# Performance work log

Hardware: AMD Instinct MI355X
Metric: run time of the kernel (lower is better)

## Reference

```python
import jax, jax.numpy as jnp
import numpy as np

N = 100000      # total nodes (100 graphs x 1000 nodes each)
G = 100         # graphs per batch
F_IN = 12       # node_features (temporal window)
F_OUT = 32      # DCRNN hidden size (hardcoded in module)
K = 5           # diffusion (Chebyshev) steps (hardcoded)
C = 4           # num_classes
E = 16 * N      # edges: ring (N) + random (15N)


def setup_inputs() -> dict:
    key = jax.random.key(0)
    ks = jax.random.split(key, 12)
    x = jax.random.normal(ks[0], (N, F_IN), dtype=jnp.float32)
    ring = jnp.arange(N, dtype=jnp.int32)
    src = jnp.concatenate([ring, jax.random.randint(ks[1], (15 * N,), 0, N, dtype=jnp.int32)])
    dst = jnp.concatenate([(ring + 1) % N, jax.random.randint(ks[2], (15 * N,), 0, N, dtype=jnp.int32)])
    edge_index = jnp.stack([src, dst])  # [2, E]
    edge_weight = jax.random.uniform(ks[3], (E,), dtype=jnp.float32, minval=0.1, maxval=1.0)
    batch = (jnp.arange(N, dtype=jnp.int32) * G) // N  # sorted graph ids, 1000 nodes per graph
    s = 0.1
    return dict(
        x=x, edge_index=edge_index, edge_weight=edge_weight, batch=batch,
        W_z=jax.random.normal(ks[4], (2, K, F_IN + F_OUT, F_OUT), jnp.float32) * s,
        b_z=jax.random.normal(ks[5], (F_OUT,), jnp.float32) * s,
        W_r=jax.random.normal(ks[6], (2, K, F_IN + F_OUT, F_OUT), jnp.float32) * s,
        b_r=jax.random.normal(ks[7], (F_OUT,), jnp.float32) * s,
        W_h=jax.random.normal(ks[8], (2, K, F_IN + F_OUT, F_OUT), jnp.float32) * s,
        b_h=jax.random.normal(ks[9], (F_OUT,), jnp.float32) * s,
        W_lin=jax.random.normal(ks[10], (F_OUT, C), jnp.float32) * s,
        b_lin=jax.random.normal(ks[11], (C,), jnp.float32) * s,
    )


def reference(x, edge_index, edge_weight, batch, W_z, b_z, W_r, b_r, W_h, b_h, W_lin, b_lin):
    row, col = edge_index[0], edge_index[1]
    # weighted in/out degrees (to_dense_adj sums duplicate edges, same as segment_sum)
    deg_out_inv = 1.0 / jax.ops.segment_sum(edge_weight, row, num_segments=N)
    deg_in_inv = 1.0 / jax.ops.segment_sum(edge_weight, col, num_segments=N)
    norm_out = deg_out_inv[row][:, None]  # per-edge 1/deg_out(src)
    norm_in = deg_in_inv[row][:, None]    # per-edge 1/deg_in(src), as in DConv

    def prop_fwd(h):  # out[dst] += h[src]/deg_out[src]
        return jax.ops.segment_sum(norm_out * h[row], col, num_segments=N)

    def prop_rev(h):  # reverse (transposed) diffusion: out[src] += h[dst]/deg_in[src]
        return jax.ops.segment_sum(norm_in * h[col], row, num_segments=N)

    def dconv(Xc, W, b):
        # Chebyshev diffusion conv, W: [2, K, F_in+F_out, F_out]
        H = Xc @ (W[0, 0] + W[1, 0])
        T1o, T1i = prop_fwd(Xc), prop_rev(Xc)
        H = H + T1o @ W[0, 1] + T1i @ W[1, 1]
        T0o = T0i = Xc
        for k in range(2, K):
            T2o = 2.0 * prop_fwd(T1o) - T0o
            T2i = 2.0 * prop_rev(T1i) - T0i
            H = H + T2o @ W[0, k] + T2i @ W[1, k]
            T0o, T1o = T1o, T2o
            T0i, T1i = T1i, T2i
        return H + b

    # GRU gating with zero-initialized hidden state (H=None in module)
    Hst = jnp.zeros((N, F_OUT), x.dtype)
    XH = jnp.concatenate([x, Hst], axis=1)
    Z = jax.nn.sigmoid(dconv(XH, W_z, b_z))
    R = jax.nn.sigmoid(dconv(XH, W_r, b_r))
    XRH = jnp.concatenate([x, R * Hst], axis=1)
    H_tilde = jnp.tanh(dconv(XRH, W_h, b_h))
    H = Z * Hst + (1.0 - Z) * H_tilde

    h = jax.nn.relu(H) @ W_lin + b_lin            # [N, C]
    sums = jax.ops.segment_sum(h, batch, num_segments=G)
    counts = jax.ops.segment_sum(jnp.ones((N,), h.dtype), batch, num_segments=G)
    return sums / counts[:, None]                 # global_mean_pool -> [G, C]
```

## Files before the change

kernel.cpp:

```cpp
#include <hip/hip_runtime.h>
#include <math.h>

#define NN    100000
#define GG    100
#define FIN   12
#define FOUT  32
#define KD    5
#define CC    4
#define EE    1600000
#define ROWS  108
#define NBF   782
#define NBINS 1564
#define NBC   256
#define CHUNK 6250
#define NSEG  (NBINS * NBC)

__device__ __forceinline__ unsigned bfr(float f) {
    unsigned u = __float_as_uint(f);
    return (u + 0x7FFFu + ((u >> 16) & 1u)) >> 16;
}
__device__ __forceinline__ unsigned pack2(float a, float b) {
    return bfr(a) | (bfr(b) << 16);
}
#define BLO(u) __uint_as_float((u) << 16)
#define BHI(u) __uint_as_float((u) & 0xFFFF0000u)

__device__ __forceinline__ int chunk_of_block(int b) {
    return ((b & 7) << 5) | (b >> 3);
}


__global__ __launch_bounds__(512) void k_hist(const int* __restrict__ ei,
                                              int* __restrict__ hist_g) {
    __shared__ int hist[NBINS];
    for (int i = threadIdx.x; i < NBINS; i += 512) hist[i] = 0;
    __syncthreads();
    int chunk = chunk_of_block(blockIdx.x);
    int lo = chunk * CHUNK, hi = lo + CHUNK;
    if (hi > EE) hi = EE;
    for (int e = lo + threadIdx.x; e < hi; e += 512) {
        int s = ei[e], d = ei[EE + e];
        atomicAdd(&hist[d >> 7], 1);
        atomicAdd(&hist[NBF + (s >> 7)], 1);
    }
    __syncthreads();
    for (int i = threadIdx.x; i < NBINS; i += 512)
        hist_g[i * NBC + chunk] = hist[i];
}

__global__ __launch_bounds__(1024) void k_scan1(int* __restrict__ g,
                                                int* __restrict__ bsum) {
    __shared__ int sh[1024];
    int t = threadIdx.x;
    int i = blockIdx.x * 1024 + t;
    int v = g[i];
    sh[t] = v;
    __syncthreads();
    for (int d = 1; d < 1024; d <<= 1) {
        int x = sh[t];
        if (t >= d) x += sh[t - d];
        __syncthreads();
        sh[t] = x;
        __syncthreads();
    }
    g[i] = sh[t] - v;
    if (t == 1023) bsum[blockIdx.x] = sh[1023];
}

__global__ __launch_bounds__(1024) void k_scan2(int* __restrict__ bsum, int nb) {
    __shared__ int sh[1024];
    int t = threadIdx.x;
    int a = (2 * t     < nb) ? bsum[2 * t]     : 0;
    int b = (2 * t + 1 < nb) ? bsum[2 * t + 1] : 0;
    int s = a + b;
    sh[t] = s;
    __syncthreads();
    for (int d = 1; d < 1024; d <<= 1) {
        int x = sh[t];
        if (t >= d) x += sh[t - d];
        __syncthreads();
        sh[t] = x;
        __syncthreads();
    }
    int base = sh[t] - s;
    if (2 * t < nb)     bsum[2 * t] = base;
    if (2 * t + 1 < nb) bsum[2 * t + 1] = base + a;
}

__global__ __launch_bounds__(1024) void k_scan3(int* __restrict__ g,
                                                const int* __restrict__ bsum,
                                                int* __restrict__ off,
                                                int* __restrict__ off_node) {
    int i = blockIdx.x * 1024 + threadIdx.x;
    int v = g[i] + bsum[blockIdx.x];
    g[i] = v;
    if ((i & (NBC - 1)) == 0) off[i / NBC] = v;
    if (i == 0) { off[NBINS] = 2 * EE; off_node[2 * NN] = 2 * EE; }
}

__global__ __launch_bounds__(512) void k_place(const int* __restrict__ ei,
                                               const float* __restrict__ ew,
                                               const int* __restrict__ base_g,
                                               int2* __restrict__ recA) {
    __shared__ int cur[NBINS];
    int chunk = chunk_of_block(blockIdx.x);
    for (int i = threadIdx.x; i < NBINS; i += 512) cur[i] = base_g[i * NBC + chunk];
    __syncthreads();
    int lo = chunk * CHUNK, hi = lo + CHUNK;
    if (hi > EE) hi = EE;
    for (int e = lo + threadIdx.x; e < hi; e += 512) {
        int s = ei[e], d = ei[EE + e];
        float w = ew[e];
        int pf = atomicAdd(&cur[d >> 7], 1);
        recA[pf] = make_int2(s | ((d & 127) << 17), __float_as_int(w));
        int pr = atomicAdd(&cur[NBF + (s >> 7)], 1);
        recA[pr] = make_int2(d | ((s & 127) << 17), __float_as_int(w));
    }
}

__global__ __launch_bounds__(256) void k_subcsr(
        const int* __restrict__ off, const int2* __restrict__ recA,
        const float* __restrict__ x,
        int* __restrict__ off_node, int* __restrict__ rec2,
        float* __restrict__ dinv_in, float* __restrict__ dinv_out,
        uint2* __restrict__ gA) {
    __shared__ int   hist[128];
    __shared__ int   lofs[128];
    __shared__ int   cur[128];
    __shared__ float wsum[128];
    __shared__ float dl[128];
    int b = blockIdx.x;
    int t = threadIdx.x;
    if (t < 128) { hist[t] = 0; wsum[t] = 0.f; }
    __syncthreads();
    int e0 = off[b], e1 = off[b + 1];
    for (int e = e0 + t; e < e1; e += 256) {
        int2 r = recA[e];
        int loc = r.x >> 17;
        atomicAdd(&hist[loc], 1);
        atomicAdd(&wsum[loc], __int_as_float(r.y));
    }
    __syncthreads();
    if (t < 128) lofs[t] = hist[t];
    __syncthreads();
    for (int d = 1; d < 128; d <<= 1) {
        int v = 0;
        if (t < 128 && t >= d) v = lofs[t - d];
        __syncthreads();
        if (t < 128) lofs[t] += v;
        __syncthreads();
    }
    bool rev = b >= NBF;
    int base = (rev ? b - NBF : b) * 128;
    if (t < 128) {
        int ex = lofs[t] - hist[t];
        lofs[t] = ex;
        cur[t] = 0;
        int node = base + t;
        if (node < NN) {
            off_node[(rev ? NN : 0) + node] = e0 + ex;
            float inv = 1.f / wsum[t];
            dl[t] = inv;
            if (rev) dinv_out[node] = inv;
            else     dinv_in[node]  = inv;
        }
    }
    __syncthreads();
    for (int e = e0 + t; e < e1; e += 256) {
        int rx = recA[e].x;
        int loc = rx >> 17;
        int pos = e0 + lofs[loc] + atomicAdd(&cur[loc], 1);
        rec2[pos] = rx & 0x1FFFF;
    }
    if (rev) {
        __syncthreads();
        for (int i = t; i < 128 * 3; i += 256) {
            int loc = i / 3, cc = i - loc * 3;
            int node = base + loc;
            if (node < NN) {
                float4 v = *(const float4*)(x + (size_t)node * FIN + cc * 4);
                float sc = dl[loc];
                gA[(size_t)node * 3 + cc] =
                    make_uint2(pack2(v.x * sc, v.y * sc), pack2(v.z * sc, v.w * sc));
            }
        }
    }
}


__global__ void k_misc(const float* __restrict__ Wz_in, const float* __restrict__ Wh_in,
                       float* __restrict__ Wz, float* __restrict__ Wh,
                       const float* __restrict__ b_lin, float* __restrict__ out,
                       const float* __restrict__ x, uint2* __restrict__ xb) {
    int t = blockIdx.x * 256 + threadIdx.x;
    if (t < 2 * ROWS * FOUT) {
        int sel = t / (ROWS * FOUT);
        int rem = t - sel * ROWS * FOUT;
        int r = rem / FOUT;
        int f = rem - r * FOUT;
        int b = r / 12;
        int i = r - b * 12;
        const float* Ws = sel ? Wh_in : Wz_in;
        float v;
        if (b == 0)
            v = Ws[(0 * KD + 0) * 44 * 32 + i * 32 + f] + Ws[(1 * KD + 0) * 44 * 32 + i * 32 + f];
        else if (b <= 4)
            v = Ws[(0 * KD + b) * 44 * 32 + i * 32 + f];
        else
            v = Ws[(1 * KD + (b - 4)) * 44 * 32 + i * 32 + f];
        (sel ? Wh : Wz)[r * FOUT + f] = v;
    }
    int u = t - 2 * ROWS * FOUT;
    if (u >= 0 && u < GG * CC) out[u] = b_lin[u & 3];
    if (t < 3 * NN) {
        int n = t / 3, c = t - n * 3;
        float4 v = *(const float4*)(x + (size_t)n * FIN + c * 4);
        xb[(size_t)n * 3 + c] = make_uint2(pack2(v.x, v.y), pack2(v.z, v.w));
    }
}

#define LREC 2048
__global__ __launch_bounds__(256) void k_gather(
        const int* __restrict__ off_node, const int* __restrict__ rec2,
        const uint2* __restrict__ gIn, const uint2* __restrict__ hIn,
        const uint2* __restrict__ prevF, const uint2* __restrict__ prevR,
        const float* __restrict__ dinv_in, const float* __restrict__ dinv_out,
        uint2* __restrict__ outF, uint2* __restrict__ outR,
        uint2* __restrict__ gOut, float c) {
    __shared__ int lrec[LREC];
    int xcd = blockIdx.x & 7;
    int grp = blockIdx.x >> 3;
    bool rev = xcd >= 4;
    int dbase = rev ? NN : 0;
    int ub = (grp * 4 + (xcd & 3)) * 256;
    int lin = ub + threadIdx.x;

    int u1 = ub + 255; if (u1 > 3 * NN - 1) u1 = 3 * NN - 1;
    int node0 = ub / 3, node1 = u1 / 3;
    int w0 = off_node[dbase + node0];
    int w1 = off_node[dbase + node1 + 1];
    int wn = w1 - w0;
    bool useLds = (wn <= LREC);
    if (useLds) {
        for (int i = threadIdx.x; i < wn; i += 256) lrec[i] = rec2[w0 + i];
    }
    __syncthreads();

    if (lin < 3 * NN) {
        int node = lin / 3;
        int ch = lin - node * 3;
        int i0 = dbase + node;
        int e0 = off_node[i0], e1 = off_node[i0 + 1];
        const uint2* in = rev ? hIn : gIn;

        float ax = 0.f, ay = 0.f, az = 0.f, aw = 0.f;
        float bx = 0.f, by = 0.f, bz = 0.f, bw = 0.f;
        if (useLds) {
            int a0 = e0 - w0, a1 = e1 - w0;
            int e = a0;
            for (; e + 7 < a1; e += 8) {
                int n0 = lrec[e],     n1 = lrec[e + 1], n2 = lrec[e + 2], n3 = lrec[e + 3];
                int n4 = lrec[e + 4], n5 = lrec[e + 5], n6 = lrec[e + 6], n7 = lrec[e + 7];
                uint2 v0 = in[(size_t)n0 * 3 + ch];
                uint2 v1 = in[(size_t)n1 * 3 + ch];
                uint2 v2 = in[(size_t)n2 * 3 + ch];
                uint2 v3 = in[(size_t)n3 * 3 + ch];
                uint2 v4 = in[(size_t)n4 * 3 + ch];
                uint2 v5 = in[(size_t)n5 * 3 + ch];
                uint2 v6 = in[(size_t)n6 * 3 + ch];
                uint2 v7 = in[(size_t)n7 * 3 + ch];
                ax += BLO(v0.x); ay += BHI(v0.x); az += BLO(v0.y); aw += BHI(v0.y);
                bx += BLO(v1.x); by += BHI(v1.x); bz += BLO(v1.y); bw += BHI(v1.y);
                ax += BLO(v2.x); ay += BHI(v2.x); az += BLO(v2.y); aw += BHI(v2.y);
                bx += BLO(v3.x); by += BHI(v3.x); bz += BLO(v3.y); bw += BHI(v3.y);
                ax += BLO(v4.x); ay += BHI(v4.x); az += BLO(v4.y); aw += BHI(v4.y);
                bx += BLO(v5.x); by += BHI(v5.x); bz += BLO(v5.y); bw += BHI(v5.y);
                ax += BLO(v6.x); ay += BHI(v6.x); az += BLO(v6.y); aw += BHI(v6.y);
                bx += BLO(v7.x); by += BHI(v7.x); bz += BLO(v7.y); bw += BHI(v7.y);
            }
            for (; e < a1; ++e) {
                int n0 = lrec[e];
                uint2 v0 = in[(size_t)n0 * 3 + ch];
                ax += BLO(v0.x); ay += BHI(v0.x); az += BLO(v0.y); aw += BHI(v0.y);
            }
        } else {
            for (int e = e0; e < e1; ++e) {
                int n0 = rec2[e];
                uint2 v0 = in[(size_t)n0 * 3 + ch];
                ax += BLO(v0.x); ay += BHI(v0.x); az += BLO(v0.y); aw += BHI(v0.y);
            }
        }
        ax += bx; ay += by; az += bz; aw += bw;

        float sc = rev ? c * dinv_in[node] : c;
        ax *= sc; ay *= sc; az *= sc; aw *= sc;

        size_t o = (size_t)node * 3 + ch;
        if (prevF) {
            uint2 p = (rev ? prevR : prevF)[o];
            ax -= BLO(p.x); ay -= BHI(p.x); az -= BLO(p.y); aw -= BHI(p.y);
        }
        (rev ? outR : outF)[o] = make_uint2(pack2(ax, ay), pack2(az, aw));
        if (!rev && gOut) {
            float g = dinv_out[node];
            gOut[o] = make_uint2(pack2(g * ax, g * ay), pack2(g * az, g * aw));
        }
    }
}


__global__ __launch_bounds__(256) void k_fused(
        const float* __restrict__ x, const uint2* __restrict__ TS2,
        const float* __restrict__ Wz, const float* __restrict__ Wh,
        const float* __restrict__ bz, const float* __restrict__ bh,
        const float* __restrict__ Wlin, float* __restrict__ out) {
    __shared__ float rows[128][13];
    __shared__ float red[256 * CC];
    int g = blockIdx.x >> 3;
    int seg = blockIdx.x & 7;
    int base = g * 1000 + seg * 125;
    int tid = threadIdx.x;
    int lane = tid & 63;
    int wave = tid >> 6;
    int f0 = __builtin_amdgcn_readfirstlane(wave * 8);

    float az0[8], ah0[8], az1[8], ah1[8];
#pragma unroll
    for (int fi = 0; fi < 8; ++fi) {
        float vz = bz[f0 + fi], vh = bh[f0 + fi];
        az0[fi] = vz; ah0[fi] = vh; az1[fi] = vz; ah1[fi] = vh;
    }
    bool act1 = (lane + 64) < 125;

    for (int b = 0; b < 9; ++b) {
        __syncthreads();
        if (b == 0) {
            const float* src = x + (size_t)base * FIN;
            for (int q = tid; q < 375; q += 256) {
                float4 v = *(const float4*)(src + q * 4);
                int e = q * 4;
                int n0 = e / 12,       i0 = e - n0 * 12;       rows[n0][i0] = v.x;
                int n1 = (e + 1) / 12, i1 = (e + 1) - n1 * 12; rows[n1][i1] = v.y;
                int n2 = (e + 2) / 12, i2 = (e + 2) - n2 * 12; rows[n2][i2] = v.z;
                int n3 = (e + 3) / 12, i3 = (e + 3) - n3 * 12; rows[n3][i3] = v.w;
            }
        } else {
            const uint2* Tb = TS2 + (size_t)(b - 1) * NN * 3;
            for (int q = tid; q < 375; q += 256) {
                int n = q / 3, cc = q - n * 3;
                uint2 v = Tb[(size_t)(base + n) * 3 + cc];
                rows[n][cc * 4 + 0] = BLO(v.x);
                rows[n][cc * 4 + 1] = BHI(v.x);
                rows[n][cc * 4 + 2] = BLO(v.y);
                rows[n][cc * 4 + 3] = BHI(v.y);
            }
        }
        __syncthreads();
        const float* wzr = Wz + b * 12 * FOUT + f0;
        const float* whr = Wh + b * 12 * FOUT + f0;
#pragma unroll
        for (int i = 0; i < FIN; ++i) {
            float v0 = rows[lane][i];
            float v1 = rows[lane + 64][i];
#pragma unroll
            for (int fi = 0; fi < 8; ++fi) {
                float wz = wzr[i * FOUT + fi];
                float wh = whr[i * FOUT + fi];
                az0[fi] = fmaf(v0, wz, az0[fi]);
                az1[fi] = fmaf(v1, wz, az1[fi]);
                ah0[fi] = fmaf(v0, wh, ah0[fi]);
                ah1[fi] = fmaf(v1, wh, ah1[fi]);
            }
        }
    }

    float o[CC] = {0.f, 0.f, 0.f, 0.f};
#pragma unroll
    for (int fi = 0; fi < 8; ++fi) {
        float z = 1.f / (1.f + __expf(-az0[fi]));
        float e2 = __expf(2.f * ah0[fi]);
        float th = 1.f - 2.f / (e2 + 1.f);
        float hv = fmaxf((1.f - z) * th, 0.f);
#pragma unroll
        for (int c = 0; c < CC; ++c) o[c] = fmaf(hv, Wlin[(f0 + fi) * 4 + c], o[c]);
    }
    if (act1) {
#pragma unroll
        for (int fi = 0; fi < 8; ++fi) {
            float z = 1.f / (1.f + __expf(-az1[fi]));
            float e2 = __expf(2.f * ah1[fi]);
            float th = 1.f - 2.f / (e2 + 1.f);
            float hv = fmaxf((1.f - z) * th, 0.f);
#pragma unroll
            for (int c = 0; c < CC; ++c) o[c] = fmaf(hv, Wlin[(f0 + fi) * 4 + c], o[c]);
        }
    }

#pragma unroll
    for (int c = 0; c < CC; ++c) red[tid * CC + c] = o[c];
    __syncthreads();
    for (int st = 128; st > 0; st >>= 1) {
        if (tid < st) {
#pragma unroll
            for (int c = 0; c < CC; ++c) red[tid * CC + c] += red[(tid + st) * CC + c];
        }
        __syncthreads();
    }
    if (tid == 0) {
#pragma unroll
        for (int c = 0; c < CC; ++c) atomicAdd(out + g * CC + c, red[c] * 0.001f);
    }
}


extern "C" void kernel_launch(void* const* d_in, const int* in_sizes, int n_in,
                              void* d_out, int out_size, void* d_ws, size_t ws_size,
                              hipStream_t stream) {
    const float* x     = (const float*)d_in[0];
    const int*   ei    = (const int*)d_in[1];
    const float* ew    = (const float*)d_in[2];
    const float* W_z   = (const float*)d_in[4];
    const float* b_z   = (const float*)d_in[5];
    const float* W_h   = (const float*)d_in[8];
    const float* b_h   = (const float*)d_in[9];
    const float* W_lin = (const float*)d_in[10];
    const float* b_lin = (const float*)d_in[11];
    float* out = (float*)d_out;

    int*   rec2     = (int*)d_ws;
    unsigned* TSb   = (unsigned*)(rec2 + 2 * (size_t)EE);
    int2*  recA     = (int2*)TSb;
    int*   hist_g   = rec2;
    int*   bsumS    = rec2 + NSEG;
    unsigned* gAu   = TSb + (size_t)8 * NN * 6 + 1600000;
    unsigned* gBu   = gAu + (size_t)NN * 6;
    unsigned* xbu   = gBu + (size_t)NN * 6;
    float* dinv_in  = (float*)(xbu + (size_t)NN * 6);
    float* dinv_out = dinv_in + NN;
    float* Wz       = dinv_out + NN;
    float* Wh       = Wz + ROWS * FOUT;
    int*   off      = (int*)(Wh + ROWS * FOUT);
    int*   off_node = off + NBINS + 1;

    uint2* TS2 = (uint2*)TSb;
    uint2* T1o = TS2 + (size_t)0 * NN * 3;
    uint2* T2o = TS2 + (size_t)1 * NN * 3;
    uint2* T3o = TS2 + (size_t)2 * NN * 3;
    uint2* T4o = TS2 + (size_t)3 * NN * 3;
    uint2* T1i = TS2 + (size_t)4 * NN * 3;
    uint2* T2i = TS2 + (size_t)5 * NN * 3;
    uint2* T3i = TS2 + (size_t)6 * NN * 3;
    uint2* T4i = TS2 + (size_t)7 * NN * 3;
    uint2* gA = (uint2*)gAu;
    uint2* gB = (uint2*)gBu;
    uint2* xb = (uint2*)xbu;

    dim3 B(256);
    int nbG = 2344;
    int nbScan = NSEG / 1024;
    int nbMisc = (3 * NN + 255) / 256;

    k_hist<<<NBC, 512, 0, stream>>>(ei, hist_g);
    k_scan1<<<nbScan, 1024, 0, stream>>>(hist_g, bsumS);
    k_scan2<<<1, 1024, 0, stream>>>(bsumS, nbScan);
    k_scan3<<<nbScan, 1024, 0, stream>>>(hist_g, bsumS, off, off_node);
    k_place<<<NBC, 512, 0, stream>>>(ei, ew, hist_g, recA);
    k_subcsr<<<NBINS, B, 0, stream>>>(off, recA, x, off_node, rec2, dinv_in, dinv_out, gA);

    k_misc<<<nbMisc, B, 0, stream>>>(W_z, W_h, Wz, Wh, b_lin, out, x, xb);

    k_gather<<<nbG, B, 0, stream>>>(off_node, rec2, gA, xb,  nullptr, nullptr, dinv_in, dinv_out, T1o, T1i, gB, 1.f);
    k_gather<<<nbG, B, 0, stream>>>(off_node, rec2, gB, T1i, xb,      xb,      dinv_in, dinv_out, T2o, T2i, gA, 2.f);
    k_gather<<<nbG, B, 0, stream>>>(off_node, rec2, gA, T2i, T1o,     T1i,     dinv_in, dinv_out, T3o, T3i, gB, 2.f);
    k_gather<<<nbG, B, 0, stream>>>(off_node, rec2, gB, T3i, T2o,     T2i,     dinv_in, dinv_out, T4o, T4i, nullptr, 2.f);

    k_fused<<<8 * GG, B, 0, stream>>>(x, TS2, Wz, Wh, b_z, b_h, W_lin, out);
}
```

Baseline: 299.0 us.

## Stage edge records in LDS per chunk before coalesced scatter to bins

Doubles the number of edge chunks, halving the edges per block. The placement kernel now sorts each chunk's records into per-bin order in shared memory, using a block-wide prefix scan of bin counts. It then writes them out contiguously per bin, replacing scattered 8-byte global writes with mostly sequential runs. This adds scan and LDS traffic plus more blocks and histogram entries in the hist/scan stages.

```diff
diff --git a/kernel.cpp b/kernel.cpp
--- a/kernel.cpp
+++ b/kernel.cpp
@@ -11,8 +11,9 @@
 #define ROWS  108
 #define NBF   782
 #define NBINS 1564
-#define NBC   256
-#define CHUNK 6250
+#define NBC   512
+#define CHUNK 3125
+#define TOTR  (2 * CHUNK)
 #define NSEG  (NBINS * NBC)
 
 __device__ __forceinline__ unsigned bfr(float f) {
@@ -26,7 +27,7 @@
 #define BHI(u) __uint_as_float((u) & 0xFFFF0000u)
 
 __device__ __forceinline__ int chunk_of_block(int b) {
-    return ((b & 7) << 5) | (b >> 3);
+    return ((b & 7) << 6) | (b >> 3);
 }
 
 
@@ -37,7 +38,6 @@
     __syncthreads();
     int chunk = chunk_of_block(blockIdx.x);
     int lo = chunk * CHUNK, hi = lo + CHUNK;
-    if (hi > EE) hi = EE;
     for (int e = lo + threadIdx.x; e < hi; e += 512) {
         int s = ei[e], d = ei[EE + e];
         atomicAdd(&hist[d >> 7], 1);
@@ -102,19 +102,69 @@
                                                const float* __restrict__ ew,
                                                const int* __restrict__ base_g,
                                                int2* __restrict__ recA) {
-    __shared__ int cur[NBINS];
+    __shared__ int2 ldsrec[TOTR];
+    __shared__ int  lofs[NBINS];
+    __shared__ int  cur[NBINS];
+    __shared__ int  sbase[NBINS];
+    __shared__ unsigned short binof[TOTR];
+    int* psum = (int*)binof;
+    int t = threadIdx.x;
     int chunk = chunk_of_block(blockIdx.x);
-    for (int i = threadIdx.x; i < NBINS; i += 512) cur[i] = base_g[i * NBC + chunk];
-    __syncthreads();
-    int lo = chunk * CHUNK, hi = lo + CHUNK;
-    if (hi > EE) hi = EE;
-    for (int e = lo + threadIdx.x; e < hi; e += 512) {
-        int s = ei[e], d = ei[EE + e];
+
+    for (int bin = t; bin < NBINS; bin += 512) {
+        int b0 = base_g[bin * NBC + chunk];
+        int b1;
+        if (chunk < NBC - 1)      b1 = base_g[bin * NBC + chunk + 1];
+        else if (bin < NBINS - 1) b1 = base_g[(bin + 1) * NBC];
+        else                      b1 = 2 * EE;
+        sbase[bin] = b0;
+        lofs[bin] = b1 - b0;
+        cur[bin] = 0;
+    }
+    __syncthreads();
+
+    int i0 = t * 4;
+    int v0 = 0, v1 = 0, v2 = 0, v3 = 0;
+    if (i0 + 0 < NBINS) v0 = lofs[i0];
+    if (i0 + 1 < NBINS) v1 = lofs[i0 + 1];
+    if (i0 + 2 < NBINS) v2 = lofs[i0 + 2];
+    if (i0 + 3 < NBINS) v3 = lofs[i0 + 3];
+    int s = v0 + v1 + v2 + v3;
+    psum[t] = s;
+    __syncthreads();
+    for (int d = 1; d < 512; d <<= 1) {
+        int x = psum[t];
+        if (t >= d) x += psum[t - d];
+        __syncthreads();
+        psum[t] = x;
+        __syncthreads();
+    }
+    int run = psum[t] - s;
+    __syncthreads();
+    if (i0 + 0 < NBINS) { lofs[i0]     = run; run += v0; }
+    if (i0 + 1 < NBINS) { lofs[i0 + 1] = run; run += v1; }
+    if (i0 + 2 < NBINS) { lofs[i0 + 2] = run; run += v2; }
+    if (i0 + 3 < NBINS) { lofs[i0 + 3] = run; run += v3; }
+    __syncthreads();
+
+    int lo = chunk * CHUNK;
+    for (int e = lo + t; e < lo + CHUNK; e += 512) {
+        int s2 = ei[e], d2 = ei[EE + e];
         float w = ew[e];
-        int pf = atomicAdd(&cur[d >> 7], 1);
-        recA[pf] = make_int2(s | ((d & 127) << 17), __float_as_int(w));
-        int pr = atomicAdd(&cur[NBF + (s >> 7)], 1);
-        recA[pr] = make_int2(d | ((s & 127) << 17), __float_as_int(w));
+        int bf = d2 >> 7;
+        int pf = lofs[bf] + atomicAdd(&cur[bf], 1);
+        ldsrec[pf] = make_int2(s2 | ((d2 & 127) << 17), __float_as_int(w));
+        binof[pf] = (unsigned short)bf;
+        int br = NBF + (s2 >> 7);
+        int pr = lofs[br] + atomicAdd(&cur[br], 1);
+        ldsrec[pr] = make_int2(d2 | ((s2 & 127) << 17), __float_as_int(w));
+        binof[pr] = (unsigned short)br;
+    }
+    __syncthreads();
+
+    for (int i = t; i < TOTR; i += 512) {
+        int b = binof[i];
+        recA[sbase[b] + (i - lofs[b])] = ldsrec[i];
     }
 }
 
```

Measured after the change: 290.2 us. 1.03x faster.
